# Kernel optimization log

Hardware: AMD Instinct MI355X
Metric: run time of the kernel (lower is better)

## Reference

```python
import jax, jax.numpy as jnp
import numpy as np

NUM_SPLITS = 4
SPLIT_CH = 4          # 16 channels / 4 splits
N_BRANCH = NUM_SPLITS * 2   # 2 pyramid branches per group
K = 2                 # multi_frequency_compression k
MAX_U, MAX_V = 5, 5
N_CLASSES = 60
LN_EPS = 1e-5


def _conv(x, w):
    # x: [B, Cin, H, W], w: [Cout, Cin, kh, kw], SAME padding, stride 1
    return jax.lax.conv_general_dilated(
        x, w, window_strides=(1, 1), padding='SAME',
        dimension_numbers=('NCHW', 'OIHW', 'NCHW'))


def _branch(x, w3, b3, w5, b5, w7, b7):
    # one PyramidMultiScaleCNN branch: dense 3x3 -> 5x5 -> 7x7 with input re-concat
    a = jax.nn.relu(_conv(x, w3) + b3[None, :, None, None])            # [B,64,H,W]
    b = jax.nn.relu(_conv(jnp.concatenate([a, x], 1), w5) + b5[None, :, None, None])  # [B,128,H,W]
    c = jax.nn.relu(_conv(jnp.concatenate([b, x], 1), w7) + b7[None, :, None, None])  # [B,256,H,W]
    return jnp.concatenate([a, b, c], axis=1)                          # [B,448,H,W]


def _dct_basis(H, W, dtype):
    # first K frequency pairs (u,v) in row-major order of a MAX_U x MAX_V grid
    uv = [(i // MAX_V, i % MAX_V) for i in range(K)]
    u = jnp.array([p[0] for p in uv], dtype=dtype)   # [K]
    v = jnp.array([p[1] for p in uv], dtype=dtype)   # [K]
    h = jnp.arange(H, dtype=dtype) + 0.5
    w = jnp.arange(W, dtype=dtype) + 0.5
    cos_u = jnp.cos(jnp.pi * u[:, None] * h[None, :] / H)  # [K,H]
    cos_v = jnp.cos(jnp.pi * v[:, None] * w[None, :] / W)  # [K,W]
    return cos_u, cos_v


def setup_inputs() -> dict:
    key = jax.random.key(0)
    ks = jax.random.split(key, 16)
    B, C, H, W = 16, 16, 32, 32
    s = 0.02
    x = jax.random.normal(ks[0], (B, C, H, W), jnp.float32)
    # stacked params for the 8 identical-shaped pyramid branches (index = 2*group + branch)
    w3 = jax.random.normal(ks[1], (N_BRANCH, 64, SPLIT_CH, 3, 3), jnp.float32) * s
    b3 = jnp.zeros((N_BRANCH, 64), jnp.float32)
    w5 = jax.random.normal(ks[2], (N_BRANCH, 128, 64 + SPLIT_CH, 5, 5), jnp.float32) * s
    b5 = jnp.zeros((N_BRANCH, 128), jnp.float32)
    w7 = jax.random.normal(ks[3], (N_BRANCH, 256, 128 + SPLIT_CH, 7, 7), jnp.float32) * s
    b7 = jnp.zeros((N_BRANCH, 256), jnp.float32)
    fused_c = N_BRANCH * 448  # 3584
    Wg = jax.random.normal(ks[4], (N_CLASSES, fused_c), jnp.float32) * s
    bg = jnp.zeros((N_CLASSES,), jnp.float32)
    f_dct = fused_c * K       # 7168
    gamma = jnp.ones((f_dct,), jnp.float32)
    beta = jnp.zeros((f_dct,), jnp.float32)
    Wd = jax.random.normal(ks[5], (N_CLASSES, f_dct), jnp.float32) * s
    bd = jnp.zeros((N_CLASSES,), jnp.float32)
    return {"x": x, "w3": w3, "b3": b3, "w5": w5, "b5": b5, "w7": w7, "b7": b7,
            "Wg": Wg, "bg": bg, "gamma": gamma, "beta": beta, "Wd": Wd, "bd": bd}


def reference(x, w3, b3, w5, b5, w7, b7, Wg, bg, gamma, beta, Wd, bd):
    B, C, H, W = x.shape
    # split channels into groups: [NUM_SPLITS, B, SPLIT_CH, H, W]
    parts = x.reshape(B, NUM_SPLITS, SPLIT_CH, H, W).transpose(1, 0, 2, 3, 4)
    # each group feeds 2 branches; branch index i = 2*group + branch matches fused cat order
    xg = jnp.repeat(parts, 2, axis=0)                               # [8,B,SPLIT_CH,H,W]
    outs = jax.vmap(_branch)(xg, w3, b3, w5, b5, w7, b7)            # [8,B,448,H,W]
    fused = outs.transpose(1, 0, 2, 3, 4).reshape(B, N_BRANCH * 448, H, W)  # [B,3584,H,W]

    # GAP head
    gap_feat = fused.mean(axis=(2, 3))                              # [B,3584]
    gap_pred = gap_feat @ Wg.T + bg                                 # [B,60]

    # batched multi-frequency DCT compression (replaces per-sample Python loop)
    cos_u, cos_v = _dct_basis(H, W, fused.dtype)                    # [K,H],[K,W]
    dct = jnp.einsum('bchw,kh,kw->bck', fused, cos_u, cos_v)        # [B,3584,K]
    dct = dct.reshape(B, -1)                                        # [B,7168]

    mu = dct.mean(axis=-1, keepdims=True)
    var = jnp.var(dct, axis=-1, keepdims=True)
    normed = (dct - mu) * jax.lax.rsqrt(var + LN_EPS) * gamma + beta
    # dropout omitted (eval mode)
    dct_pred = normed @ Wd.T + bd                                   # [B,60]
    return (gap_pred, dct_pred)
```

## Files before the change

kernel.cpp:

```cpp
#include <hip/hip_runtime.h>
#include <math.h>

#define PI_F 3.14159265358979323846f

typedef short bf16x8 __attribute__((ext_vector_type(8)));
typedef float f32x4  __attribute__((ext_vector_type(4)));
typedef float f32x16 __attribute__((ext_vector_type(16)));

__device__ __forceinline__ short f2bf(float f) {
    union { float f; unsigned u; } v; v.f = f;
    unsigned r = v.u + 0x7fffu + ((v.u >> 16) & 1u);
    return (short)(r >> 16);
}

__device__ __forceinline__ void gld16(const short* g, short* l) {
    __builtin_amdgcn_global_load_lds(
        (const __attribute__((address_space(1))) unsigned int*)g,
        (__attribute__((address_space(3))) unsigned int*)l, 16, 0, 0);
}


__global__ __launch_bounds__(256) void prep_s1in(const float* __restrict__ x, short* __restrict__ dst) {
    int idx = blockIdx.x * 256 + threadIdx.x;
    if (idx >= 64 * 1024) return;
    int px = idx & 1023;
    int g  = (idx >> 10) & 3;
    int b  = idx >> 12;
    short v8[8];
    #pragma unroll
    for (int j = 0; j < 8; ++j) {
        float f = (j < 4) ? x[((b * 16 + g * 4 + j) << 10) + px] : 0.f;
        v8[j] = f2bf(f);
    }
    *(int4*)(dst + (size_t)idx * 8) = *(const int4*)v8;
}

__global__ __launch_bounds__(256) void prep_sx(const float* __restrict__ x, short* __restrict__ dst,
                                               int CHS, int CH0) {
    int idx = blockIdx.x * 256 + threadIdx.x;
    if (idx >= 128 * 1024) return;
    int px = idx & 1023, pair = idx >> 10;
    int i = pair >> 4, b = pair & 15, g = i >> 1;
    short v8[8];
    #pragma unroll
    for (int j = 0; j < 8; ++j) {
        float f = (j < 4) ? x[((b * 16 + g * 4 + j) << 10) + px] : 0.f;
        v8[j] = f2bf(f);
    }
    *(int4*)(dst + (size_t)idx * CHS + CH0) = *(const int4*)v8;
}

__global__ __launch_bounds__(256) void prep_s3x(const float* __restrict__ x, short* __restrict__ dst) {
    int idx = blockIdx.x * 256 + threadIdx.x;
    if (idx >= 128 * 1024) return;
    int px = idx & 1023, pair = idx >> 10;
    int i = pair >> 4, b = pair & 15, g = i >> 1;
    int R = px >> 5, C = px & 31;
    short v8[8];
    #pragma unroll
    for (int j = 0; j < 8; ++j) {
        float f = (j < 4) ? x[((b * 16 + g * 4 + j) << 10) + px] : 0.f;
        v8[j] = f2bf(f);
    }
    int p = ((C + 3) * 136 + 128) * 2;
    p ^= ((p >> 7) & 1) << 4;
    *(int4*)((char*)dst + ((size_t)pair * 38 + R + 3) * 11264 + p) = *(const int4*)v8;
}

template<int KS, int CHS, int CINR, int COUT, int NCH>
__global__ __launch_bounds__(256) void wprep_d(const float* __restrict__ w, short* __restrict__ Bw) {
    constexpr int TOTAL = 8 * KS * NCH * COUT * 4;
    int idx = blockIdx.x * 256 + threadIdx.x;
    if (idx >= TOTAL) return;
    int kb = idx & 3;
    int r  = idx >> 2;
    int n  = r % COUT;  r /= COUT;
    int c  = r % NCH;   r /= NCH;
    int kh = r % KS;
    int br = r / KS;
    short v8[8];
    #pragma unroll
    for (int j = 0; j < 8; ++j) {
        int k   = c * 32 + kb * 8 + j;
        int kwc = k / CHS;
        int ch  = k - kwc * CHS;
        float f = (kwc < KS && ch < CINR)
                ? w[(((size_t)br * COUT + n) * CINR + ch) * (KS * KS) + kh * KS + kwc] : 0.f;
        v8[j] = f2bf(f);
    }
    *(int4*)(Bw + (size_t)idx * 8) = *(const int4*)v8;
}

__global__ __launch_bounds__(256) void wprep7c(const float* __restrict__ w, short* __restrict__ Bw) {
    __shared__ float lds[12936];
    const int t = threadIdx.x;
    const int pairN = blockIdx.x & 127;
    const int br    = blockIdx.x >> 7;
    const int n0 = pairN * 2;
    const float* src = w + ((size_t)br * 256 + n0) * 6468;
    for (int e = t; e < 3234; e += 256)
        *(float4*)(lds + e * 4) = *(const float4*)(src + e * 4);
    __syncthreads();
    for (int e = t; e < 1680; e += 256) {
        int oct = e & 3;
        int r = e >> 2;
        int c  = r % 30; r /= 30;
        int kh = r % 7;
        int dn = r / 7;
        short v8[8];
        #pragma unroll
        for (int j = 0; j < 8; ++j) {
            int k = c * 32 + oct * 8 + j;
            int kwc = k / 136, ch = k - kwc * 136;
            float f = (kwc < 7 && ch < 132) ? lds[dn * 6468 + ch * 49 + kh * 7 + kwc] : 0.f;
            v8[j] = f2bf(f);
        }
        size_t dst = ((((size_t)br * 7 + kh) * 30 + c) * 256 + (n0 + dn)) * 32 + oct * 8;
        *(int4*)(Bw + dst) = *(const int4*)v8;
    }
}

template<int KS, int CHS, int COUT, int CHS_OUT, int FOFF, bool S1SRC, bool POUT>
__global__ __launch_bounds__(512, 2) void conv_hk(
    const short* __restrict__ sIn,
    short* __restrict__ sOut,
    const short* __restrict__ Bw,
    const float* __restrict__ bias,
    float* __restrict__ sums)
{
    constexpr int PAD    = KS / 2;
    constexpr int NCH    = (KS * CHS + 31) / 32;
    constexpr int TCX    = 32 + (NCH * 32 - 1) / CHS;
    constexpr int NSLOT  = 9;
    constexpr int NFN    = COUT / 64;
    constexpr int CPP    = CHS / 8;
    constexpr int RCHK   = TCX * CPP;
    constexpr int CHUNKB = COUT * 32;
    static_assert(NCH == 1 || (NCH % 2) == 0, "NCH must be 1 or even");
    static_assert(RCHK <= 512, "single stg reg");

    __shared__ int4 AtileV[(NSLOT * TCX * CHS) / 8];
    short* Atile = (short*)AtileV;

    const int t    = threadIdx.x;
    const int lane = t & 63, w = t >> 6;
    const int wm = w >> 2, wn = w & 3;
    const int lm = lane & 15, kb = lane >> 4;

    const int bid = blockIdx.x;
    const int i  = bid & 7;
    const int b  = (bid >> 3) & 15;
    const int mt = bid >> 7;
    const int r0 = mt * 8;

    const int pairIdx = i * 16 + b;
    const int pairPx = pairIdx << 10;
    const int srcPx  = S1SRC ? ((b * 4 + (i >> 1)) << 10) : pairPx;

    int nIdx[NFN], nOff[NFN];
    #pragma unroll
    for (int fn = 0; fn < NFN; ++fn) {
        nIdx[fn] = wn * (COUT / 4) + fn * 16 + lm;
        nOff[fn] = nIdx[fn] * 32 + kb * 8;
    }

    f32x4 acc[8][NFN];
    #pragma unroll
    for (int fm = 0; fm < 8; ++fm)
        #pragma unroll
        for (int fn = 0; fn < NFN; ++fn)
            acc[fm][fn] = (f32x4){0.f, 0.f, 0.f, 0.f};

    const short* Bp = Bw + (size_t)i * KS * NCH * CHUNKB;
    bf16x8 b0[NFN], b1[NFN];
    #pragma unroll
    for (int fn = 0; fn < NFN; ++fn)
        b0[fn] = *(const bf16x8*)(Bp + nOff[fn]);

    for (int e = t; e < 9 * RCHK; e += 512) {
        int j  = e / RCHK, e2 = e - j * RCHK;
        int tc = e2 / CPP, kc = e2 - tc * CPP;
        int rin = r0 - PAD + j, cin = tc - PAD;
        int4 v = {0, 0, 0, 0};
        if (rin >= 0 && rin < 32 && cin >= 0 && cin < 32)
            v = *(const int4*)(sIn + (size_t)(srcPx + rin * 32 + cin) * CHS + kc * 8);
        *(int4*)(Atile + (j * TCX + tc) * CHS + kc * 8) = v;
    }
    __syncthreads();

    int aB[8];

    for (int kh = 0; kh < KS; ++kh) {
        #pragma unroll
        for (int fm = 0; fm < 8; ++fm) {
            int slot = kh + wm * 4 + (fm >> 1);
            if (slot >= NSLOT) slot -= NSLOT;
            aB[fm] = (slot * TCX + (fm & 1) * 16 + lm) * CHS + kb * 8;
        }

        const bool doStage = (kh <= KS - 3);
        const int stRin = r0 - PAD + kh + 9;
        int4 stg0 = {0, 0, 0, 0};
        if (doStage) {
            if (t < RCHK) {
                int tc = t / CPP, kc = t - tc * CPP;
                int cin = tc - PAD;
                if (stRin >= 0 && stRin < 32 && cin >= 0 && cin < 32)
                    stg0 = *(const int4*)(sIn + (size_t)(srcPx + stRin * 32 + cin) * CHS + kc * 8);
            }
        }

        if constexpr (NCH == 1) {
            __builtin_amdgcn_s_setprio(1);
            #pragma unroll
            for (int fm = 0; fm < 8; ++fm) {
                bf16x8 af = *(const bf16x8*)(Atile + aB[fm]);
                #pragma unroll
                for (int fn = 0; fn < NFN; ++fn)
                    acc[fm][fn] = __builtin_amdgcn_mfma_f32_16x16x32_bf16(af, b0[fn], acc[fm][fn], 0, 0, 0);
            }
            __builtin_amdgcn_s_setprio(0);
            if (kh < KS - 1) {
                #pragma unroll
                for (int fn = 0; fn < NFN; ++fn)
                    b0[fn] = *(const bf16x8*)(Bp + CHUNKB + nOff[fn]);
            }
            Bp += CHUNKB;
        } else {
            #pragma unroll 1
            for (int c = 0; c < NCH; c += 2) {
                #pragma unroll
                for (int fn = 0; fn < NFN; ++fn)
                    b1[fn] = *(const bf16x8*)(Bp + (size_t)(c + 1) * CHUNKB + nOff[fn]);
                __builtin_amdgcn_s_setprio(1);
                #pragma unroll
                for (int fm = 0; fm < 8; ++fm) {
                    bf16x8 af = *(const bf16x8*)(Atile + aB[fm] + c * 32);
                    #pragma unroll
                    for (int fn = 0; fn < NFN; ++fn)
                        acc[fm][fn] = __builtin_amdgcn_mfma_f32_16x16x32_bf16(af, b0[fn], acc[fm][fn], 0, 0, 0);
                }
                __builtin_amdgcn_s_setprio(0);
                if (!(kh == KS - 1 && c + 2 >= NCH)) {
                    #pragma unroll
                    for (int fn = 0; fn < NFN; ++fn)
                        b0[fn] = *(const bf16x8*)(Bp + (size_t)(c + 2) * CHUNKB + nOff[fn]);
                }
                __builtin_amdgcn_s_setprio(1);
                #pragma unroll
                for (int fm = 0; fm < 8; ++fm) {
                    bf16x8 af = *(const bf16x8*)(Atile + aB[fm] + (c + 1) * 32);
                    #pragma unroll
                    for (int fn = 0; fn < NFN; ++fn)
                        acc[fm][fn] = __builtin_amdgcn_mfma_f32_16x16x32_bf16(af, b1[fn], acc[fm][fn], 0, 0, 0);
                }
                __builtin_amdgcn_s_setprio(0);
            }
            Bp += (size_t)NCH * CHUNKB;
        }

        __syncthreads();
        if (doStage && t < RCHK) {
            int tc = t / CPP, kc = t - tc * CPP;
            *(int4*)(Atile + (kh * TCX + tc) * CHS + kc * 8) = stg0;
        }
    }

    float cwv[2][4];
    #pragma unroll
    for (int half = 0; half < 2; ++half)
        #pragma unroll
        for (int r = 0; r < 4; ++r)
            cwv[half][r] = cosf(PI_F * (half * 16 + kb * 4 + r + 0.5f) / 32.f);

    #pragma unroll
    for (int fn = 0; fn < NFN; ++fn) {
        int n = nIdx[fn];
        float bv = bias[i * COUT + n];
        float s0 = 0.f, s1 = 0.f;
        #pragma unroll
        for (int fm = 0; fm < 8; ++fm) {
            int imgrow = wm * 4 + (fm >> 1);
            int half = fm & 1;
            #pragma unroll
            for (int r = 0; r < 4; ++r) {
                float v = fmaxf(acc[fm][fn][r] + bv, 0.f);
                int col = half * 16 + kb * 4 + r;
                int R = r0 + imgrow;
                if constexpr (POUT) {
                    int p = ((col + 3) * CHS_OUT + n) * 2;
                    p ^= ((p >> 7) & 1) << 4;
                    *(short*)((char*)sOut + ((size_t)pairIdx * 38 + R + 3) * 11264 + p) = f2bf(v);
                } else if constexpr (CHS_OUT > 0) {
                    sOut[(size_t)(pairPx + R * 32 + col) * CHS_OUT + n] = f2bf(v);
                }
                s0 += v;
                s1 += v * cwv[half][r];
            }
        }
        s0 += __shfl_xor(s0, 16); s1 += __shfl_xor(s1, 16);
        s0 += __shfl_xor(s0, 32); s1 += __shfl_xor(s1, 32);
        if (kb == 0) {
            int ch = i * 448 + FOFF + n;
            atomicAdd(&sums[((size_t)b * 3584 + ch) * 2 + 0], s0);
            atomicAdd(&sums[((size_t)b * 3584 + ch) * 2 + 1], s1);
        }
    }
}

__global__ __launch_bounds__(512, 2) void conv7_fused(
    const short* __restrict__ sPad,
    const short* __restrict__ Bw,
    const float* __restrict__ bias,
    float* __restrict__ sums)
{
    constexpr int NCH = 30, COUT = 256;
    constexpr int RSTR = 5632;
    constexpr int CHUNKB = COUT * 32;

    __shared__ int4 AldsV[(14 * RSTR) / 8];
    short* Alds = (short*)AldsV;

    const int t    = threadIdx.x;
    const int lane = t & 63, w = t >> 6;
    const int ln = lane & 31, hi = lane >> 5;

    const int bid = blockIdx.x;
    const int i  = bid & 7;
    const int b  = (bid >> 3) & 15;
    const int mt = bid >> 7;
    const int r0 = mt * 8;
    const size_t sBase = (size_t)(i * 16 + b) * 38 * RSTR;

    const int n = w * 32 + ln;
    const int nOffB = n * 32 + hi * 8;

    f32x16 acc[8];
    #pragma unroll
    for (int ro = 0; ro < 8; ++ro) acc[ro] = (f32x16)(0.f);

    const short* BpI = Bw + (size_t)i * 7 * NCH * CHUNKB;

    for (int s = w; s < 154; s += 8) {
        int j = s / 11, sg = s - j * 11;
        gld16(sPad + sBase + (size_t)(r0 + j) * RSTR + sg * 512 + lane * 8,
              Alds + j * RSTR + sg * 512 + lane * 8);
    }
    bf16x8 bA[7], bB[7];
    #pragma unroll
    for (int kh = 0; kh < 7; ++kh)
        bA[kh] = *(const bf16x8*)(BpI + (size_t)kh * NCH * CHUNKB + nOffB);
    __syncthreads();

    auto HALF = [&](bf16x8 (&bq)[7], int c, int kk) {
        int swb = ln * 272 + c * 64 + kk * 32 + hi * 16;
        swb ^= ((swb >> 7) & 1) << 4;
        #pragma unroll
        for (int j = 0; j < 14; ++j) {
            bf16x8 af = *(const bf16x8*)((const char*)Alds + j * 11264 + swb);
            const int klo = (j > 7) ? (j - 7) : 0;
            const int khi = (j < 6) ? j : 6;
            #pragma unroll
            for (int kh = klo; kh <= khi; ++kh)
                acc[j - kh] = __builtin_amdgcn_mfma_f32_32x32x16_bf16(af, bq[kh], acc[j - kh], 0, 0, 0);
        }
    };

    #pragma unroll 1
    for (int c = 0; c < NCH; ++c) {
        #pragma unroll
        for (int kh = 0; kh < 7; ++kh)
            bB[kh] = *(const bf16x8*)(BpI + ((size_t)kh * NCH + c) * CHUNKB + nOffB + 16);
        HALF(bA, c, 0);
        if (c + 1 < NCH) {
            #pragma unroll
            for (int kh = 0; kh < 7; ++kh)
                bA[kh] = *(const bf16x8*)(BpI + ((size_t)kh * NCH + c + 1) * CHUNKB + nOffB);
        }
        HALF(bB, c, 1);
    }

    float cw[16];
    #pragma unroll
    for (int r = 0; r < 16; ++r) {
        int px = (r & 3) + 8 * (r >> 2) + 4 * hi;
        cw[r] = cosf(PI_F * (px + 0.5f) / 32.f);
    }

    float bv = bias[i * COUT + n];
    float s0 = 0.f, s1 = 0.f;
    #pragma unroll
    for (int ro = 0; ro < 8; ++ro) {
        #pragma unroll
        for (int r = 0; r < 16; ++r) {
            float v = fmaxf(acc[ro][r] + bv, 0.f);
            s0 += v;
            s1 += v * cw[r];
        }
    }
    s0 += __shfl_xor(s0, 32);
    s1 += __shfl_xor(s1, 32);
    if (hi == 0) {
        int ch = i * 448 + 192 + n;
        atomicAdd(&sums[((size_t)b * 3584 + ch) * 2 + 0], s0);
        atomicAdd(&sums[((size_t)b * 3584 + ch) * 2 + 1], s1);
    }
}

__global__ __launch_bounds__(256) void ln_stats(const float* __restrict__ sums,
                                                float* __restrict__ stats) {
    __shared__ float red[8];
    const int b = blockIdx.x;
    const int t = threadIdx.x, lane = t & 63, wv = t >> 6;
    const float* S = sums + (size_t)b * 7168;
    float ls = 0.f, lq = 0.f;
    for (int f = t; f < 7168; f += 256) { float v = S[f]; ls += v; lq += v * v; }
    for (int m = 1; m < 64; m <<= 1) { ls += __shfl_xor(ls, m); lq += __shfl_xor(lq, m); }
    if (lane == 0) { red[wv] = ls; red[4 + wv] = lq; }
    __syncthreads();
    if (t == 0) {
        float ts = red[0] + red[1] + red[2] + red[3];
        float tq = red[4] + red[5] + red[6] + red[7];
        float mu  = ts * (1.f / 7168.f);
        float var = tq * (1.f / 7168.f) - mu * mu;
        stats[b * 2 + 0] = mu;
        stats[b * 2 + 1] = rsqrtf(var + 1e-5f);
    }
}

__global__ __launch_bounds__(256) void head_gemv(
    const float* __restrict__ sums,
    const float* __restrict__ stats,
    const float* __restrict__ Wg, const float* __restrict__ bg,
    const float* __restrict__ gamma, const float* __restrict__ beta,
    const float* __restrict__ Wd, const float* __restrict__ bd,
    float* __restrict__ out)
{
    __shared__ float red[8];
    const int n = blockIdx.x % 60;
    const int b = blockIdx.x / 60;
    const int t = threadIdx.x, lane = t & 63, wv = t >> 6;
    const float* S  = sums + (size_t)b * 7168;
    const float mu  = stats[b * 2 + 0];
    const float inv = stats[b * 2 + 1];

    const float* wd = Wd + (size_t)n * 7168;
    float accd = 0.f;
    for (int f = t; f < 7168; f += 256) {
        float v = (S[f] - mu) * inv * gamma[f] + beta[f];
        accd = fmaf(v, wd[f], accd);
    }
    const float* wg = Wg + (size_t)n * 3584;
    float accg = 0.f;
    for (int ch = t; ch < 3584; ch += 256)
        accg = fmaf(S[2 * ch], wg[ch], accg);

    for (int m = 1; m < 64; m <<= 1) { accg += __shfl_xor(accg, m); accd += __shfl_xor(accd, m); }
    if (lane == 0) { red[wv] = accg; red[4 + wv] = accd; }
    __syncthreads();
    if (t == 0) {
        float g = red[0] + red[1] + red[2] + red[3];
        float d = red[4] + red[5] + red[6] + red[7];
        out[b * 60 + n]       = g * (1.f / 1024.f) + bg[n];
        out[960 + b * 60 + n] = d + bd[n];
    }
}

extern "C" void kernel_launch(void* const* d_in, const int* in_sizes, int n_in,
                              void* d_out, int out_size, void* d_ws, size_t ws_size,
                              hipStream_t stream)
{
    const float* x     = (const float*)d_in[0];
    const float* w3    = (const float*)d_in[1];
    const float* b3    = (const float*)d_in[2];
    const float* w5    = (const float*)d_in[3];
    const float* b5    = (const float*)d_in[4];
    const float* w7    = (const float*)d_in[5];
    const float* b7    = (const float*)d_in[6];
    const float* Wg    = (const float*)d_in[7];
    const float* bg    = (const float*)d_in[8];
    const float* gamma = (const float*)d_in[9];
    const float* beta  = (const float*)d_in[10];
    const float* Wd    = (const float*)d_in[11];
    const float* bd    = (const float*)d_in[12];
    float* out = (float*)d_out;

    char* p = (char*)d_ws;
    float* sums  = (float*)p;             p += 458752;
    float* stats = (float*)p;             p += 128;
    short* s1in  = (short*)p;             p += 1048576;
    short* s2in  = (short*)p;             p += 18874368;
    short* s3pad = (short*)p;             p += 54788096;
    short* Bw3   = (short*)p;             p += 98304;
    short* Bw5   = (short*)p;             p += 3932160;
    short* Bw7   = (short*)p;             p += 27525120;

    hipMemsetAsync(sums, 0, 458752, stream);
    hipMemsetAsync(s3pad, 0, 54788096, stream);
    prep_s1in<<<dim3(256), dim3(256), 0, stream>>>(x, s1in);
    prep_sx<<<dim3(512), dim3(256), 0, stream>>>(x, s2in, 72, 64);
    prep_s3x<<<dim3(512), dim3(256), 0, stream>>>(x, s3pad);
    wprep_d<3, 8, 4, 64, 1><<<dim3(24), dim3(256), 0, stream>>>(w3, Bw3);
    wprep_d<5, 72, 68, 128, 12><<<dim3(960), dim3(256), 0, stream>>>(w5, Bw5);
    wprep7c<<<dim3(1024), dim3(256), 0, stream>>>(w7, Bw7);

    conv_hk<3, 8, 64, 72, 0, true, false><<<dim3(512), dim3(512), 0, stream>>>(s1in, s2in, Bw3, b3, sums);
    conv_hk<5, 72, 128, 136, 64, false, true><<<dim3(512), dim3(512), 0, stream>>>(s2in, s3pad, Bw5, b5, sums);
    conv7_fused<<<dim3(512), dim3(512), 0, stream>>>(s3pad, Bw7, b7, sums);

    ln_stats<<<dim3(16), dim3(256), 0, stream>>>(sums, stats);
    head_gemv<<<dim3(960), dim3(256), 0, stream>>>(sums, stats, Wg, bg, gamma, beta, Wd, bd, out);
}
```

Before: 450.5 us.

## Add dedicated 5x5 conv kernel using padded swizzled input and 32x32 MFMA

Replaces the generic conv_hk 5x5 path with conv5_fused. The new kernel loads a padded, swizzled 20-row input tile into LDS through direct global-to-LDS loads and accumulates 16 output rows per block with 32x32x16 MFMAs, reusing each A fragment across the five kh taps. The 3x3 conv and the input prep now write into a padded s2 layout, which costs an extra memset. The s2 buffer shares workspace with Bw7, so the 7x7 weight prep is moved after conv5. The grid for the 5x5 stage is halved to 256 blocks, which risks lower occupancy.

Result: slower. 467.7 us (+3.8%).

```diff
diff --git a/kernel.cpp b/kernel.cpp
--- a/kernel.cpp
+++ b/kernel.cpp
@@ -35,19 +35,21 @@
     *(int4*)(dst + (size_t)idx * 8) = *(const int4*)v8;
 }
 
-__global__ __launch_bounds__(256) void prep_sx(const float* __restrict__ x, short* __restrict__ dst,
-                                               int CHS, int CH0) {
+__global__ __launch_bounds__(256) void prep_s2x(const float* __restrict__ x, short* __restrict__ dst) {
     int idx = blockIdx.x * 256 + threadIdx.x;
     if (idx >= 128 * 1024) return;
     int px = idx & 1023, pair = idx >> 10;
     int i = pair >> 4, b = pair & 15, g = i >> 1;
+    int R = px >> 5, C = px & 31;
     short v8[8];
     #pragma unroll
     for (int j = 0; j < 8; ++j) {
         float f = (j < 4) ? x[((b * 16 + g * 4 + j) << 10) + px] : 0.f;
         v8[j] = f2bf(f);
     }
-    *(int4*)(dst + (size_t)idx * CHS + CH0) = *(const int4*)v8;
+    int p = ((C + 2) * 72 + 64) * 2;
+    p ^= ((p >> 7) & 1) << 4;
+    *(int4*)((char*)dst + ((size_t)pair * 36 + R + 2) * 5632 + p) = *(const int4*)v8;
 }
 
 __global__ __launch_bounds__(256) void prep_s3x(const float* __restrict__ x, short* __restrict__ dst) {
@@ -120,7 +122,7 @@
     }
 }
 
-template<int KS, int CHS, int COUT, int CHS_OUT, int FOFF, bool S1SRC, bool POUT>
+template<int KS, int CHS, int COUT, int FOFF, bool S1SRC>
 __global__ __launch_bounds__(512, 2) void conv_hk(
     const short* __restrict__ sIn,
     short* __restrict__ sOut,
@@ -136,8 +138,7 @@
     constexpr int CPP    = CHS / 8;
     constexpr int RCHK   = TCX * CPP;
     constexpr int CHUNKB = COUT * 32;
-    static_assert(NCH == 1 || (NCH % 2) == 0, "NCH must be 1 or even");
-    static_assert(RCHK <= 512, "single stg reg");
+    static_assert(NCH == 1, "conv3 path");
 
     __shared__ int4 AtileV[(NSLOT * TCX * CHS) / 8];
     short* Atile = (short*)AtileV;
@@ -154,8 +155,7 @@
     const int r0 = mt * 8;
 
     const int pairIdx = i * 16 + b;
-    const int pairPx = pairIdx << 10;
-    const int srcPx  = S1SRC ? ((b * 4 + (i >> 1)) << 10) : pairPx;
+    const int srcPx  = S1SRC ? ((b * 4 + (i >> 1)) << 10) : (pairIdx << 10);
 
     int nIdx[NFN], nOff[NFN];
     #pragma unroll
@@ -172,7 +172,7 @@
             acc[fm][fn] = (f32x4){0.f, 0.f, 0.f, 0.f};
 
     const short* Bp = Bw + (size_t)i * KS * NCH * CHUNKB;
-    bf16x8 b0[NFN], b1[NFN];
+    bf16x8 b0[NFN];
     #pragma unroll
     for (int fn = 0; fn < NFN; ++fn)
         b0[fn] = *(const bf16x8*)(Bp + nOff[fn]);
@@ -189,7 +189,6 @@
     __syncthreads();
 
     int aB[8];
-
     for (int kh = 0; kh < KS; ++kh) {
         #pragma unroll
         for (int fm = 0; fm < 8; ++fm) {
@@ -201,63 +200,28 @@
         const bool doStage = (kh <= KS - 3);
         const int stRin = r0 - PAD + kh + 9;
         int4 stg0 = {0, 0, 0, 0};
-        if (doStage) {
-            if (t < RCHK) {
-                int tc = t / CPP, kc = t - tc * CPP;
-                int cin = tc - PAD;
-                if (stRin >= 0 && stRin < 32 && cin >= 0 && cin < 32)
-                    stg0 = *(const int4*)(sIn + (size_t)(srcPx + stRin * 32 + cin) * CHS + kc * 8);
-            }
-        }
-
-        if constexpr (NCH == 1) {
-            __builtin_amdgcn_s_setprio(1);
-            #pragma unroll
-            for (int fm = 0; fm < 8; ++fm) {
-                bf16x8 af = *(const bf16x8*)(Atile + aB[fm]);
-                #pragma unroll
-                for (int fn = 0; fn < NFN; ++fn)
-                    acc[fm][fn] = __builtin_amdgcn_mfma_f32_16x16x32_bf16(af, b0[fn], acc[fm][fn], 0, 0, 0);
-            }
-            __builtin_amdgcn_s_setprio(0);
-            if (kh < KS - 1) {
-                #pragma unroll
-                for (int fn = 0; fn < NFN; ++fn)
-                    b0[fn] = *(const bf16x8*)(Bp + CHUNKB + nOff[fn]);
-            }
-            Bp += CHUNKB;
-        } else {
-            #pragma unroll 1
-            for (int c = 0; c < NCH; c += 2) {
-                #pragma unroll
-                for (int fn = 0; fn < NFN; ++fn)
-                    b1[fn] = *(const bf16x8*)(Bp + (size_t)(c + 1) * CHUNKB + nOff[fn]);
-                __builtin_amdgcn_s_setprio(1);
-                #pragma unroll
-                for (int fm = 0; fm < 8; ++fm) {
-                    bf16x8 af = *(const bf16x8*)(Atile + aB[fm] + c * 32);
-                    #pragma unroll
-                    for (int fn = 0; fn < NFN; ++fn)
-                        acc[fm][fn] = __builtin_amdgcn_mfma_f32_16x16x32_bf16(af, b0[fn], acc[fm][fn], 0, 0, 0);
-                }
-                __builtin_amdgcn_s_setprio(0);
-                if (!(kh == KS - 1 && c + 2 >= NCH)) {
-                    #pragma unroll
-                    for (int fn = 0; fn < NFN; ++fn)
-                        b0[fn] = *(const bf16x8*)(Bp + (size_t)(c + 2) * CHUNKB + nOff[fn]);
-                }
-                __builtin_amdgcn_s_setprio(1);
-                #pragma unroll
-                for (int fm = 0; fm < 8; ++fm) {
-                    bf16x8 af = *(const bf16x8*)(Atile + aB[fm] + (c + 1) * 32);
-                    #pragma unroll
-                    for (int fn = 0; fn < NFN; ++fn)
-                        acc[fm][fn] = __builtin_amdgcn_mfma_f32_16x16x32_bf16(af, b1[fn], acc[fm][fn], 0, 0, 0);
-                }
-                __builtin_amdgcn_s_setprio(0);
-            }
-            Bp += (size_t)NCH * CHUNKB;
-        }
+        if (doStage && t < RCHK) {
+            int tc = t / CPP, kc = t - tc * CPP;
+            int cin = tc - PAD;
+            if (stRin >= 0 && stRin < 32 && cin >= 0 && cin < 32)
+                stg0 = *(const int4*)(sIn + (size_t)(srcPx + stRin * 32 + cin) * CHS + kc * 8);
+        }
+
+        __builtin_amdgcn_s_setprio(1);
+        #pragma unroll
+        for (int fm = 0; fm < 8; ++fm) {
+            bf16x8 af = *(const bf16x8*)(Atile + aB[fm]);
+            #pragma unroll
+            for (int fn = 0; fn < NFN; ++fn)
+                acc[fm][fn] = __builtin_amdgcn_mfma_f32_16x16x32_bf16(af, b0[fn], acc[fm][fn], 0, 0, 0);
+        }
+        __builtin_amdgcn_s_setprio(0);
+        if (kh < KS - 1) {
+            #pragma unroll
+            for (int fn = 0; fn < NFN; ++fn)
+                b0[fn] = *(const bf16x8*)(Bp + CHUNKB + nOff[fn]);
+        }
+        Bp += CHUNKB;
 
         __syncthreads();
         if (doStage && t < RCHK) {
@@ -287,13 +251,9 @@
                 float v = fmaxf(acc[fm][fn][r] + bv, 0.f);
                 int col = half * 16 + kb * 4 + r;
                 int R = r0 + imgrow;
-                if constexpr (POUT) {
-                    int p = ((col + 3) * CHS_OUT + n) * 2;
-                    p ^= ((p >> 7) & 1) << 4;
-                    *(short*)((char*)sOut + ((size_t)pairIdx * 38 + R + 3) * 11264 + p) = f2bf(v);
-                } else if constexpr (CHS_OUT > 0) {
-                    sOut[(size_t)(pairPx + R * 32 + col) * CHS_OUT + n] = f2bf(v);
-                }
+                int p = ((col + 2) * 72 + n) * 2;
+                p ^= ((p >> 7) & 1) << 4;
+                *(short*)((char*)sOut + ((size_t)pairIdx * 36 + R + 2) * 5632 + p) = f2bf(v);
                 s0 += v;
                 s1 += v * cwv[half][r];
             }
@@ -305,6 +265,111 @@
             atomicAdd(&sums[((size_t)b * 3584 + ch) * 2 + 0], s0);
             atomicAdd(&sums[((size_t)b * 3584 + ch) * 2 + 1], s1);
         }
+    }
+}
+
+__global__ __launch_bounds__(512, 2) void conv5_fused(
+    const short* __restrict__ s2pad,
+    short* __restrict__ s3pad,
+    const short* __restrict__ Bw,
+    const float* __restrict__ bias,
+    float* __restrict__ sums)
+{
+    constexpr int NCH = 12, COUT = 128;
+    constexpr int RS2 = 2816;
+    constexpr int CHUNKB = COUT * 32;
+
+    __shared__ int4 AldsV[(20 * RS2) / 8];
+    short* Alds = (short*)AldsV;
+
+    const int t = threadIdx.x;
+    const int lane = t & 63, w = t >> 6;
+    const int Mg = w >> 2, ns = w & 3;
+    const int ln = lane & 31, hi = lane >> 5;
+
+    const int bid = blockIdx.x;
+    const int i  = bid & 7;
+    const int b  = (bid >> 3) & 15;
+    const int mt = bid >> 7;
+    const int pairIdx = i * 16 + b;
+
+    const int n = ns * 32 + ln;
+    const int nOffB = n * 32 + hi * 8;
+
+    f32x16 acc[8];
+    #pragma unroll
+    for (int d = 0; d < 8; ++d) acc[d] = (f32x16)(0.f);
+
+    const short* BpI = Bw + (size_t)i * 5 * NCH * CHUNKB;
+    bf16x8 bA[5], bB[5];
+    #pragma unroll
+    for (int kh = 0; kh < 5; ++kh)
+        bA[kh] = *(const bf16x8*)(BpI + (size_t)kh * NCH * CHUNKB + nOffB);
+
+    const short* src = s2pad + ((size_t)pairIdx * 36 + mt * 16) * RS2;
+    for (int s = w; s < 110; s += 8)
+        gld16(src + s * 512 + lane * 8, Alds + s * 512 + lane * 8);
+    __syncthreads();
+
+    const char* Abase = (const char*)Alds + Mg * 8 * 5632;
+
+    auto HALF = [&](bf16x8 (&bq)[5], int c, int kk) {
+        int swb = ln * 144 + c * 64 + kk * 32 + hi * 16;
+        swb ^= ((swb >> 7) & 1) << 4;
+        #pragma unroll
+        for (int jp = 0; jp < 12; ++jp) {
+            bf16x8 af = *(const bf16x8*)(Abase + jp * 5632 + swb);
+            const int klo = (jp > 7) ? (jp - 7) : 0;
+            const int khi = (jp < 4) ? jp : 4;
+            #pragma unroll
+            for (int kh = klo; kh <= khi; ++kh)
+                acc[jp - kh] = __builtin_amdgcn_mfma_f32_32x32x16_bf16(af, bq[kh], acc[jp - kh], 0, 0, 0);
+        }
+    };
+
+    #pragma unroll 1
+    for (int c = 0; c < NCH; ++c) {
+        #pragma unroll
+        for (int kh = 0; kh < 5; ++kh)
+            bB[kh] = *(const bf16x8*)(BpI + ((size_t)kh * NCH + c) * CHUNKB + nOffB + 16);
+        HALF(bA, c, 0);
+        if (c + 1 < NCH) {
+            #pragma unroll
+            for (int kh = 0; kh < 5; ++kh)
+                bA[kh] = *(const bf16x8*)(BpI + ((size_t)kh * NCH + c + 1) * CHUNKB + nOffB);
+        }
+        HALF(bB, c, 1);
+    }
+
+    float cw[16];
+    #pragma unroll
+    for (int r = 0; r < 16; ++r) {
+        int px = (r & 3) + 8 * (r >> 2) + 4 * hi;
+        cw[r] = cosf(PI_F * (px + 0.5f) / 32.f);
+    }
+
+    float bv = bias[i * COUT + n];
+    float s0 = 0.f, s1 = 0.f;
+    #pragma unroll
+    for (int d = 0; d < 8; ++d) {
+        int R = mt * 16 + Mg * 8 + d;
+        #pragma unroll
+        for (int r = 0; r < 16; ++r) {
+            float v = fmaxf(acc[d][r] + bv, 0.f);
+            int px = (r & 3) + 8 * (r >> 2) + 4 * hi;
+            int p = ((px + 3) * 136 + n) * 2;
+            p ^= ((p >> 7) & 1) << 4;
+            *(short*)((char*)s3pad + ((size_t)pairIdx * 38 + R + 3) * 11264 + p) = f2bf(v);
+            s0 += v;
+            s1 += v * cw[r];
+        }
+    }
+    s0 += __shfl_xor(s0, 32);
+    s1 += __shfl_xor(s1, 32);
+    if (hi == 0) {
+        int ch = i * 448 + 64 + n;
+        atomicAdd(&sums[((size_t)b * 3584 + ch) * 2 + 0], s0);
+        atomicAdd(&sums[((size_t)b * 3584 + ch) * 2 + 1], s1);
     }
 }
 
@@ -489,23 +554,24 @@
     float* sums  = (float*)p;             p += 458752;
     float* stats = (float*)p;             p += 128;
     short* s1in  = (short*)p;             p += 1048576;
-    short* s2in  = (short*)p;             p += 18874368;
+    short* s2pad = (short*)p;
+    short* Bw7   = (short*)p;             p += 27525120;
     short* s3pad = (short*)p;             p += 54788096;
     short* Bw3   = (short*)p;             p += 98304;
     short* Bw5   = (short*)p;             p += 3932160;
-    short* Bw7   = (short*)p;             p += 27525120;
 
     hipMemsetAsync(sums, 0, 458752, stream);
+    hipMemsetAsync(s2pad, 0, 25952256, stream);
     hipMemsetAsync(s3pad, 0, 54788096, stream);
     prep_s1in<<<dim3(256), dim3(256), 0, stream>>>(x, s1in);
-    prep_sx<<<dim3(512), dim3(256), 0, stream>>>(x, s2in, 72, 64);
+    prep_s2x<<<dim3(512), dim3(256), 0, stream>>>(x, s2pad);
     prep_s3x<<<dim3(512), dim3(256), 0, stream>>>(x, s3pad);
     wprep_d<3, 8, 4, 64, 1><<<dim3(24), dim3(256), 0, stream>>>(w3, Bw3);
     wprep_d<5, 72, 68, 128, 12><<<dim3(960), dim3(256), 0, stream>>>(w5, Bw5);
+
+    conv_hk<3, 8, 64, 0, true><<<dim3(512), dim3(512), 0, stream>>>(s1in, s2pad, Bw3, b3, sums);
+    conv5_fused<<<dim3(256), dim3(512), 0, stream>>>(s2pad, s3pad, Bw5, b5, sums);
     wprep7c<<<dim3(1024), dim3(256), 0, stream>>>(w7, Bw7);
-
-    conv_hk<3, 8, 64, 72, 0, true, false><<<dim3(512), dim3(512), 0, stream>>>(s1in, s2in, Bw3, b3, sums);
-    conv_hk<5, 72, 128, 136, 64, false, true><<<dim3(512), dim3(512), 0, stream>>>(s2in, s3pad, Bw5, b5, sums);
     conv7_fused<<<dim3(512), dim3(512), 0, stream>>>(s3pad, Bw7, b7, sums);
 
     ln_stats<<<dim3(16), dim3(256), 0, stream>>>(sums, stats);
```
